# Kernel tuning notes

Measured on AMD Instinct MI355X. Metric: run time of the kernel, lower is better.

The kernel has to match this reference:

```python
import jax, jax.numpy as jnp
import numpy as np

N_NODES = 100000
N_EDGES = 1600000
D_FEAT = 64


def setup_inputs() -> dict:
    key = jax.random.key(0)
    k1, k2 = jax.random.split(key)
    x = jax.random.normal(k1, (N_NODES, D_FEAT), dtype=jnp.float32)
    edge_index = jax.random.randint(k2, (2, N_EDGES), 0, N_NODES, dtype=jnp.int64)
    return {"x": x, "edge_index": edge_index}


def reference(x, edge_index):
    # GCNProp (improved=False): remove self loops, add self loops w/ weight 1,
    # symmetric deg^-1/2 normalization, then spmm aggregation.
    N = x.shape[0]
    row, col = edge_index[0], edge_index[1]
    # remove_self_loops: zero the weight of any self-loop edge (math-equivalent
    # to dropping it, and jit-friendly: no data-dependent shapes).
    w = jnp.where(row != col, jnp.ones((), x.dtype), jnp.zeros((), x.dtype))
    # add_self_loops: append N diagonal edges with loop_value = 1 (improved=False)
    loop = jnp.arange(N, dtype=row.dtype)
    row_a = jnp.concatenate([row, loop])          # [E+N]
    col_a = jnp.concatenate([col, loop])          # [E+N]
    w_a = jnp.concatenate([w, jnp.ones((N,), x.dtype)])  # [E+N]
    # degree via scatter_add over rows
    deg = jax.ops.segment_sum(w_a, row_a, num_segments=N)  # [N]
    # deg^-0.5 with inf -> 0
    dinv = jnp.where(deg > 0, jax.lax.rsqrt(deg), jnp.zeros((), x.dtype))
    # edge normalization: deg[row]^-1/2 * w * deg[col]^-1/2
    norm = dinv[row_a] * w_a * dinv[col_a]        # [E+N]
    # spmm: gather neighbor features, scale, scatter-add into rows
    out = jax.ops.segment_sum(norm[:, None] * x[col_a], row_a, num_segments=N)  # [N, D]
    return out
```

## Files before the change

### kernel.cpp

```cpp
#include <hip/hip_runtime.h>

#define N_NODES 100000
#define N_EDGES 1600000
#define D 64
#define NB 391
#define BCAP 4480
#define PBLK 512
#define TPB 512
#define CHUNK ((N_EDGES + PBLK - 1) / PBLK)
#define CURSTRIDE 32

__device__ __forceinline__ unsigned short f2b(float f) {
    unsigned u = __float_as_uint(f);
    u += 0x7FFF + ((u >> 16) & 1);
    return (unsigned short)(u >> 16);
}

__global__ void init_cursor_kernel(int* __restrict__ cursor) {
    int b = blockIdx.x * blockDim.x + threadIdx.x;
    if (b < NB) cursor[b * CURSTRIDE] = b * BCAP;
}

__global__ __launch_bounds__(TPB) void scatter_direct_kernel(const int* __restrict__ ei,
                                                             int* __restrict__ cursor,
                                                             int* __restrict__ epack) {
    __shared__ int er[CHUNK];
    __shared__ int ec[CHUNK];
    __shared__ int h[NB];
    __shared__ int lbase[NB];
    __shared__ int lcur[NB];
    int t = threadIdx.x;
    for (int i = t; i < NB; i += TPB) h[i] = 0;
    int s = blockIdx.x * CHUNK;
    int e = min(s + CHUNK, N_EDGES);
    int n = e - s;
    for (int i = t; i < n; i += TPB) {
        er[i] = ei[s + i];
        ec[i] = ei[N_EDGES + s + i];
    }
    __syncthreads();
    for (int i = t; i < n; i += TPB) {
        int r = er[i], c = ec[i];
        if (r != c) atomicAdd(&h[r >> 8], 1);
    }
    __syncthreads();
    for (int i = t; i < NB; i += TPB) {
        lbase[i] = atomicAdd(&cursor[i * CURSTRIDE], h[i]);
        lcur[i] = 0;
    }
    __syncthreads();
    for (int i = t; i < n; i += TPB) {
        int r = er[i], c = ec[i];
        if (r != c) {
            int b = r >> 8;
            int p = lbase[b] + atomicAdd(&lcur[b], 1);
            epack[p] = ((r & 255) << 17) | c;
        }
    }
}

__global__ __launch_bounds__(TPB) void csr_sort_convert_kernel(const int* __restrict__ cursor,
                                                               int* __restrict__ epack,
                                                               int2* __restrict__ rowinfo,
                                                               const float* __restrict__ x,
                                                               unsigned short* __restrict__ xs) {
    __shared__ int ebuf[BCAP];
    __shared__ int h[256];
    __shared__ int sc[256];
    __shared__ int cur[256];
    __shared__ float dv[256];
    int b = blockIdx.x;
    int t = threadIdx.x;
    int base = b * BCAP;
    int n = min(cursor[b * CURSTRIDE] - base, BCAP);
    for (int i = t; i < n; i += TPB) ebuf[i] = epack[base + i];
    if (t < 256) h[t] = 0;
    __syncthreads();
    for (int i = t; i < n; i += TPB) atomicAdd(&h[ebuf[i] >> 17], 1);
    __syncthreads();
    int v = 0;
    if (t < 256) { v = h[t]; sc[t] = v; }
    __syncthreads();
    for (int off = 1; off < 256; off <<= 1) {
        int u = (t < 256 && t >= off) ? sc[t - off] : 0;
        __syncthreads();
        if (t < 256) sc[t] += u;
        __syncthreads();
    }
    if (t < 256) {
        int excl = sc[t] - v;
        int row = b * 256 + t;
        if (row < N_NODES) rowinfo[row] = make_int2(base + excl, v);
        dv[t] = rsqrtf((float)(1 + v));
        cur[t] = excl;
    }
    __syncthreads();
    for (int i = t; i < n; i += TPB) {
        int p = ebuf[i];
        int pos = atomicAdd(&cur[p >> 17], 1);
        epack[base + pos] = (p & 0x1FFFF) << 7;
    }
    int nrows = min(256, N_NODES - b * 256);
    const float4* x4 = (const float4*)x;
    ushort4* xs4 = (ushort4*)xs;
    for (int i = t; i < nrows * 16; i += TPB) {
        int rl = i >> 4;
        float4 vv = x4[(size_t)(b * 256 + rl) * 16 + (i & 15)];
        float dd = dv[rl];
        ushort4 o;
        o.x = f2b(vv.x * dd);
        o.y = f2b(vv.y * dd);
        o.z = f2b(vv.z * dd);
        o.w = f2b(vv.w * dd);
        xs4[(size_t)(b * 256 + rl) * 16 + (i & 15)] = o;
    }
}

__global__ __launch_bounds__(256) void gather_kernel(const unsigned short* __restrict__ xs,
                                                     const int2* __restrict__ rowinfo,
                                                     const int* __restrict__ colidx,
                                                     float* __restrict__ out) {
    int t = blockIdx.x * blockDim.x + threadIdx.x;
    int r = t >> 6;
    int lane = t & 63;
    if (r >= N_NODES) return;
    int lp = lane & 31;
    int hf = lane >> 5;
    int lpo = lp << 2;
    int2 ri = rowinfo[r];
    int start = ri.x;
    int end = start + ri.y;
    float dr = rsqrtf((float)(1 + ri.y));
    const char* xsb = (const char*)xs;
    float ax = 0.0f, ay = 0.0f;
    if (hf == 0) {
        unsigned v = *(const unsigned*)(xsb + (((size_t)r) << 7) + lpo);
        ax = __uint_as_float(v << 16);
        ay = __uint_as_float(v & 0xFFFF0000u);
    }
    for (int j = start; j < end; j += 64) {
        int idx = j + lane;
        int cj = (idx < end) ? colidx[idx] : 0;
        int n = min(64, end - j);
        int k = 0;
        for (; 2 * (k + 8) <= n; k += 8) {
            int s0 = __shfl(cj, 2 * k + hf);
            int s1 = __shfl(cj, 2 * k + 2 + hf);
            int s2 = __shfl(cj, 2 * k + 4 + hf);
            int s3 = __shfl(cj, 2 * k + 6 + hf);
            int s4 = __shfl(cj, 2 * k + 8 + hf);
            int s5 = __shfl(cj, 2 * k + 10 + hf);
            int s6 = __shfl(cj, 2 * k + 12 + hf);
            int s7 = __shfl(cj, 2 * k + 14 + hf);
            unsigned v0 = *(const unsigned*)(xsb + (unsigned)(s0 + lpo));
            unsigned v1 = *(const unsigned*)(xsb + (unsigned)(s1 + lpo));
            unsigned v2 = *(const unsigned*)(xsb + (unsigned)(s2 + lpo));
            unsigned v3 = *(const unsigned*)(xsb + (unsigned)(s3 + lpo));
            unsigned v4 = *(const unsigned*)(xsb + (unsigned)(s4 + lpo));
            unsigned v5 = *(const unsigned*)(xsb + (unsigned)(s5 + lpo));
            unsigned v6 = *(const unsigned*)(xsb + (unsigned)(s6 + lpo));
            unsigned v7 = *(const unsigned*)(xsb + (unsigned)(s7 + lpo));
            float a0 = __uint_as_float(v0 << 16), b0 = __uint_as_float(v0 & 0xFFFF0000u);
            float a1 = __uint_as_float(v1 << 16), b1 = __uint_as_float(v1 & 0xFFFF0000u);
            float a2 = __uint_as_float(v2 << 16), b2 = __uint_as_float(v2 & 0xFFFF0000u);
            float a3 = __uint_as_float(v3 << 16), b3 = __uint_as_float(v3 & 0xFFFF0000u);
            float a4 = __uint_as_float(v4 << 16), b4 = __uint_as_float(v4 & 0xFFFF0000u);
            float a5 = __uint_as_float(v5 << 16), b5 = __uint_as_float(v5 & 0xFFFF0000u);
            float a6 = __uint_as_float(v6 << 16), b6 = __uint_as_float(v6 & 0xFFFF0000u);
            float a7 = __uint_as_float(v7 << 16), b7 = __uint_as_float(v7 & 0xFFFF0000u);
            ax += ((a0 + a1) + (a2 + a3)) + ((a4 + a5) + (a6 + a7));
            ay += ((b0 + b1) + (b2 + b3)) + ((b4 + b5) + (b6 + b7));
        }
        for (; 2 * (k + 4) <= n; k += 4) {
            int s0 = __shfl(cj, 2 * k + hf);
            int s1 = __shfl(cj, 2 * k + 2 + hf);
            int s2 = __shfl(cj, 2 * k + 4 + hf);
            int s3 = __shfl(cj, 2 * k + 6 + hf);
            unsigned v0 = *(const unsigned*)(xsb + (unsigned)(s0 + lpo));
            unsigned v1 = *(const unsigned*)(xsb + (unsigned)(s1 + lpo));
            unsigned v2 = *(const unsigned*)(xsb + (unsigned)(s2 + lpo));
            unsigned v3 = *(const unsigned*)(xsb + (unsigned)(s3 + lpo));
            float a0 = __uint_as_float(v0 << 16), b0 = __uint_as_float(v0 & 0xFFFF0000u);
            float a1 = __uint_as_float(v1 << 16), b1 = __uint_as_float(v1 & 0xFFFF0000u);
            float a2 = __uint_as_float(v2 << 16), b2 = __uint_as_float(v2 & 0xFFFF0000u);
            float a3 = __uint_as_float(v3 << 16), b3 = __uint_as_float(v3 & 0xFFFF0000u);
            ax += (a0 + a1) + (a2 + a3);
            ay += (b0 + b1) + (b2 + b3);
        }
        for (; 2 * k < n; k++) {
            int src = 2 * k + hf;
            int s0 = __shfl(cj, (src < n) ? src : (n - 1));
            unsigned v0 = *(const unsigned*)(xsb + (unsigned)(s0 + lpo));
            if (src < n) {
                ax += __uint_as_float(v0 << 16);
                ay += __uint_as_float(v0 & 0xFFFF0000u);
            }
        }
    }
    ax += __shfl_xor(ax, 32);
    ay += __shfl_xor(ay, 32);
    if (hf == 0) {
        float2 o;
        o.x = dr * ax;
        o.y = dr * ay;
        ((float2*)out)[(size_t)r * 32 + lp] = o;
    }
}

extern "C" void kernel_launch(void* const* d_in, const int* in_sizes, int n_in,
                              void* d_out, int out_size, void* d_ws, size_t ws_size,
                              hipStream_t stream) {
    const float* x = (const float*)d_in[0];
    const int* ei = (const int*)d_in[1];
    float* out = (float*)d_out;

    int* cursor = (int*)d_ws;
    int2* rowinfo = (int2*)(cursor + NB * CURSTRIDE);
    int* epack = (int*)(rowinfo + N_NODES);
    unsigned short* xs = (unsigned short*)(epack + NB * BCAP);

    init_cursor_kernel<<<(NB + 255) / 256, 256, 0, stream>>>(cursor);
    scatter_direct_kernel<<<PBLK, TPB, 0, stream>>>(ei, cursor, epack);
    csr_sort_convert_kernel<<<NB, TPB, 0, stream>>>(cursor, epack, rowinfo, x, xs);
    gather_kernel<<<(N_NODES * D + 255) / 256, 256, 0, stream>>>(xs, rowinfo, epack, out);
}
```

Measured before the change: 160.1 us.

## Halve bucket size to 128 rows and drop LDS edge staging in scatter

Rows are now grouped into 782 buckets of 128 rows instead of 391 buckets of 256, and the sort/convert kernel runs with 256 threads per block. This gives more, smaller blocks with less shared memory each, which should raise occupancy and parallelism. The scatter kernel no longer stages edges in LDS and instead re-reads them from global memory in both passes. It also skips the global atomic for empty buckets. The trade-off is a second global read of the edge list in exchange for much lower LDS use in the scatter kernel, plus a tighter per-bucket capacity that could overflow if a bucket gets unusually many edges.

```diff
diff --git a/kernel.cpp b/kernel.cpp
--- a/kernel.cpp
+++ b/kernel.cpp
@@ -3,8 +3,9 @@
 #define N_NODES 100000
 #define N_EDGES 1600000
 #define D 64
-#define NB 391
-#define BCAP 4480
+#define BROWS 128
+#define NBK 782
+#define BCAP 2368
 #define PBLK 512
 #define TPB 512
 #define CHUNK ((N_EDGES + PBLK - 1) / PBLK)
@@ -18,101 +19,95 @@
 
 __global__ void init_cursor_kernel(int* __restrict__ cursor) {
     int b = blockIdx.x * blockDim.x + threadIdx.x;
-    if (b < NB) cursor[b * CURSTRIDE] = b * BCAP;
+    if (b < NBK) cursor[b * CURSTRIDE] = b * BCAP;
 }
 
 __global__ __launch_bounds__(TPB) void scatter_direct_kernel(const int* __restrict__ ei,
                                                              int* __restrict__ cursor,
                                                              int* __restrict__ epack) {
-    __shared__ int er[CHUNK];
-    __shared__ int ec[CHUNK];
-    __shared__ int h[NB];
-    __shared__ int lbase[NB];
-    __shared__ int lcur[NB];
+    __shared__ int h[NBK];
+    __shared__ int lbase[NBK];
+    __shared__ int lcur[NBK];
     int t = threadIdx.x;
-    for (int i = t; i < NB; i += TPB) h[i] = 0;
+    for (int i = t; i < NBK; i += TPB) h[i] = 0;
+    __syncthreads();
     int s = blockIdx.x * CHUNK;
     int e = min(s + CHUNK, N_EDGES);
-    int n = e - s;
-    for (int i = t; i < n; i += TPB) {
-        er[i] = ei[s + i];
-        ec[i] = ei[N_EDGES + s + i];
-    }
-    __syncthreads();
-    for (int i = t; i < n; i += TPB) {
-        int r = er[i], c = ec[i];
-        if (r != c) atomicAdd(&h[r >> 8], 1);
-    }
-    __syncthreads();
-    for (int i = t; i < NB; i += TPB) {
-        lbase[i] = atomicAdd(&cursor[i * CURSTRIDE], h[i]);
+    for (int i = s + t; i < e; i += TPB) {
+        int r = ei[i], c = ei[N_EDGES + i];
+        if (r != c) atomicAdd(&h[r >> 7], 1);
+    }
+    __syncthreads();
+    for (int i = t; i < NBK; i += TPB) {
+        int hv = h[i];
+        lbase[i] = hv ? atomicAdd(&cursor[i * CURSTRIDE], hv) : 0;
         lcur[i] = 0;
     }
     __syncthreads();
-    for (int i = t; i < n; i += TPB) {
-        int r = er[i], c = ec[i];
+    for (int i = s + t; i < e; i += TPB) {
+        int r = ei[i], c = ei[N_EDGES + i];
         if (r != c) {
-            int b = r >> 8;
+            int b = r >> 7;
             int p = lbase[b] + atomicAdd(&lcur[b], 1);
-            epack[p] = ((r & 255) << 17) | c;
-        }
-    }
-}
-
-__global__ __launch_bounds__(TPB) void csr_sort_convert_kernel(const int* __restrict__ cursor,
+            epack[p] = ((r & 127) << 17) | c;
+        }
+    }
+}
+
+__global__ __launch_bounds__(256) void csr_sort_convert_kernel(const int* __restrict__ cursor,
                                                                int* __restrict__ epack,
                                                                int2* __restrict__ rowinfo,
                                                                const float* __restrict__ x,
                                                                unsigned short* __restrict__ xs) {
     __shared__ int ebuf[BCAP];
-    __shared__ int h[256];
-    __shared__ int sc[256];
-    __shared__ int cur[256];
-    __shared__ float dv[256];
+    __shared__ int h[BROWS];
+    __shared__ int sc[BROWS];
+    __shared__ int cur[BROWS];
+    __shared__ float dv[BROWS];
     int b = blockIdx.x;
     int t = threadIdx.x;
     int base = b * BCAP;
     int n = min(cursor[b * CURSTRIDE] - base, BCAP);
-    for (int i = t; i < n; i += TPB) ebuf[i] = epack[base + i];
-    if (t < 256) h[t] = 0;
-    __syncthreads();
-    for (int i = t; i < n; i += TPB) atomicAdd(&h[ebuf[i] >> 17], 1);
+    for (int i = t; i < n; i += 256) ebuf[i] = epack[base + i];
+    if (t < BROWS) h[t] = 0;
+    __syncthreads();
+    for (int i = t; i < n; i += 256) atomicAdd(&h[ebuf[i] >> 17], 1);
     __syncthreads();
     int v = 0;
-    if (t < 256) { v = h[t]; sc[t] = v; }
-    __syncthreads();
-    for (int off = 1; off < 256; off <<= 1) {
-        int u = (t < 256 && t >= off) ? sc[t - off] : 0;
+    if (t < BROWS) { v = h[t]; sc[t] = v; }
+    __syncthreads();
+    for (int off = 1; off < BROWS; off <<= 1) {
+        int u = (t < BROWS && t >= off) ? sc[t - off] : 0;
         __syncthreads();
-        if (t < 256) sc[t] += u;
+        if (t < BROWS) sc[t] += u;
         __syncthreads();
     }
-    if (t < 256) {
+    if (t < BROWS) {
         int excl = sc[t] - v;
-        int row = b * 256 + t;
+        int row = b * BROWS + t;
         if (row < N_NODES) rowinfo[row] = make_int2(base + excl, v);
         dv[t] = rsqrtf((float)(1 + v));
         cur[t] = excl;
     }
     __syncthreads();
-    for (int i = t; i < n; i += TPB) {
+    for (int i = t; i < n; i += 256) {
         int p = ebuf[i];
         int pos = atomicAdd(&cur[p >> 17], 1);
         epack[base + pos] = (p & 0x1FFFF) << 7;
     }
-    int nrows = min(256, N_NODES - b * 256);
+    int nrows = min(BROWS, N_NODES - b * BROWS);
     const float4* x4 = (const float4*)x;
     ushort4* xs4 = (ushort4*)xs;
-    for (int i = t; i < nrows * 16; i += TPB) {
+    for (int i = t; i < nrows * 16; i += 256) {
         int rl = i >> 4;
-        float4 vv = x4[(size_t)(b * 256 + rl) * 16 + (i & 15)];
+        float4 vv = x4[(size_t)(b * BROWS + rl) * 16 + (i & 15)];
         float dd = dv[rl];
         ushort4 o;
         o.x = f2b(vv.x * dd);
         o.y = f2b(vv.y * dd);
         o.z = f2b(vv.z * dd);
         o.w = f2b(vv.w * dd);
-        xs4[(size_t)(b * 256 + rl) * 16 + (i & 15)] = o;
+        xs4[(size_t)(b * BROWS + rl) * 16 + (i & 15)] = o;
     }
 }
 
@@ -215,12 +210,12 @@
     float* out = (float*)d_out;
 
     int* cursor = (int*)d_ws;
-    int2* rowinfo = (int2*)(cursor + NB * CURSTRIDE);
+    int2* rowinfo = (int2*)(cursor + NBK * CURSTRIDE);
     int* epack = (int*)(rowinfo + N_NODES);
-    unsigned short* xs = (unsigned short*)(epack + NB * BCAP);
-
-    init_cursor_kernel<<<(NB + 255) / 256, 256, 0, stream>>>(cursor);
+    unsigned short* xs = (unsigned short*)(epack + NBK * BCAP);
+
+    init_cursor_kernel<<<(NBK + 255) / 256, 256, 0, stream>>>(cursor);
     scatter_direct_kernel<<<PBLK, TPB, 0, stream>>>(ei, cursor, epack);
-    csr_sort_convert_kernel<<<NB, TPB, 0, stream>>>(cursor, epack, rowinfo, x, xs);
+    csr_sort_convert_kernel<<<NBK, 256, 0, stream>>>(cursor, epack, rowinfo, x, xs);
     gather_kernel<<<(N_NODES * D + 255) / 256, 256, 0, stream>>>(xs, rowinfo, epack, out);
 }
```

Result: slower. 167.3 us (+4.5%).

## Split bf16 conversion into its own kernel and drop scatter's shared staging

Applied to the files above, without the earlier changes.

Moves the x-scaling and bf16 conversion out of the per-bucket sort kernel into a separate, more finely parallel kernel, with deg^-1/2 passed through a new dinv buffer. The scatter kernel now uses 256 blocks of 1024 threads and reads edges straight from global memory twice, where it used to stage them in shared memory. It also skips cursor atomics for empty buckets and vectorises the epack load in the sort kernel. The aim is more parallelism and less shared-memory pressure, at the cost of an extra kernel launch and a second global pass over the edges.

```diff
diff --git a/kernel.cpp b/kernel.cpp
--- a/kernel.cpp
+++ b/kernel.cpp
@@ -5,10 +5,12 @@
 #define D 64
 #define NB 391
 #define BCAP 4480
-#define PBLK 512
+#define PBLK 256
+#define STPB 1024
 #define TPB 512
 #define CHUNK ((N_EDGES + PBLK - 1) / PBLK)
 #define CURSTRIDE 32
+#define CROWS 64
 
 __device__ __forceinline__ unsigned short f2b(float f) {
     unsigned u = __float_as_uint(f);
@@ -21,36 +23,30 @@
     if (b < NB) cursor[b * CURSTRIDE] = b * BCAP;
 }
 
-__global__ __launch_bounds__(TPB) void scatter_direct_kernel(const int* __restrict__ ei,
-                                                             int* __restrict__ cursor,
-                                                             int* __restrict__ epack) {
-    __shared__ int er[CHUNK];
-    __shared__ int ec[CHUNK];
+__global__ __launch_bounds__(STPB) void scatter_direct_kernel(const int* __restrict__ ei,
+                                                              int* __restrict__ cursor,
+                                                              int* __restrict__ epack) {
     __shared__ int h[NB];
     __shared__ int lbase[NB];
     __shared__ int lcur[NB];
     int t = threadIdx.x;
-    for (int i = t; i < NB; i += TPB) h[i] = 0;
+    for (int i = t; i < NB; i += STPB) h[i] = 0;
+    __syncthreads();
     int s = blockIdx.x * CHUNK;
     int e = min(s + CHUNK, N_EDGES);
-    int n = e - s;
-    for (int i = t; i < n; i += TPB) {
-        er[i] = ei[s + i];
-        ec[i] = ei[N_EDGES + s + i];
-    }
-    __syncthreads();
-    for (int i = t; i < n; i += TPB) {
-        int r = er[i], c = ec[i];
+    for (int i = s + t; i < e; i += STPB) {
+        int r = ei[i], c = ei[N_EDGES + i];
         if (r != c) atomicAdd(&h[r >> 8], 1);
     }
     __syncthreads();
-    for (int i = t; i < NB; i += TPB) {
-        lbase[i] = atomicAdd(&cursor[i * CURSTRIDE], h[i]);
+    for (int i = t; i < NB; i += STPB) {
+        int hv = h[i];
+        lbase[i] = hv ? atomicAdd(&cursor[i * CURSTRIDE], hv) : 0;
         lcur[i] = 0;
     }
     __syncthreads();
-    for (int i = t; i < n; i += TPB) {
-        int r = er[i], c = ec[i];
+    for (int i = s + t; i < e; i += STPB) {
+        int r = ei[i], c = ei[N_EDGES + i];
         if (r != c) {
             int b = r >> 8;
             int p = lbase[b] + atomicAdd(&lcur[b], 1);
@@ -59,21 +55,22 @@
     }
 }
 
-__global__ __launch_bounds__(TPB) void csr_sort_convert_kernel(const int* __restrict__ cursor,
-                                                               int* __restrict__ epack,
-                                                               int2* __restrict__ rowinfo,
-                                                               const float* __restrict__ x,
-                                                               unsigned short* __restrict__ xs) {
+__global__ __launch_bounds__(TPB) void csr_sort_kernel(const int* __restrict__ cursor,
+                                                       int* __restrict__ epack,
+                                                       int2* __restrict__ rowinfo,
+                                                       float* __restrict__ dinv) {
     __shared__ int ebuf[BCAP];
     __shared__ int h[256];
     __shared__ int sc[256];
     __shared__ int cur[256];
-    __shared__ float dv[256];
     int b = blockIdx.x;
     int t = threadIdx.x;
     int base = b * BCAP;
     int n = min(cursor[b * CURSTRIDE] - base, BCAP);
-    for (int i = t; i < n; i += TPB) ebuf[i] = epack[base + i];
+    const int4* ep4 = (const int4*)(epack + base);
+    int n4 = n >> 2;
+    for (int i = t; i < n4; i += TPB) ((int4*)ebuf)[i] = ep4[i];
+    for (int i = (n4 << 2) + t; i < n; i += TPB) ebuf[i] = epack[base + i];
     if (t < 256) h[t] = 0;
     __syncthreads();
     for (int i = t; i < n; i += TPB) atomicAdd(&h[ebuf[i] >> 17], 1);
@@ -90,8 +87,10 @@
     if (t < 256) {
         int excl = sc[t] - v;
         int row = b * 256 + t;
-        if (row < N_NODES) rowinfo[row] = make_int2(base + excl, v);
-        dv[t] = rsqrtf((float)(1 + v));
+        if (row < N_NODES) {
+            rowinfo[row] = make_int2(base + excl, v);
+            dinv[row] = rsqrtf((float)(1 + v));
+        }
         cur[t] = excl;
     }
     __syncthreads();
@@ -100,19 +99,30 @@
         int pos = atomicAdd(&cur[p >> 17], 1);
         epack[base + pos] = (p & 0x1FFFF) << 7;
     }
-    int nrows = min(256, N_NODES - b * 256);
+}
+
+__global__ __launch_bounds__(256) void convert_kernel(const float* __restrict__ x,
+                                                      const float* __restrict__ dinv,
+                                                      unsigned short* __restrict__ xs) {
+    __shared__ float dv[CROWS];
+    int b = blockIdx.x;
+    int t = threadIdx.x;
+    int r0 = b * CROWS;
+    int nrows = min(CROWS, N_NODES - r0);
+    if (t < nrows) dv[t] = dinv[r0 + t];
+    __syncthreads();
     const float4* x4 = (const float4*)x;
     ushort4* xs4 = (ushort4*)xs;
-    for (int i = t; i < nrows * 16; i += TPB) {
+    for (int i = t; i < nrows * 16; i += 256) {
         int rl = i >> 4;
-        float4 vv = x4[(size_t)(b * 256 + rl) * 16 + (i & 15)];
+        float4 vv = x4[(size_t)(r0 + rl) * 16 + (i & 15)];
         float dd = dv[rl];
         ushort4 o;
         o.x = f2b(vv.x * dd);
         o.y = f2b(vv.y * dd);
         o.z = f2b(vv.z * dd);
         o.w = f2b(vv.w * dd);
-        xs4[(size_t)(b * 256 + rl) * 16 + (i & 15)] = o;
+        xs4[(size_t)(r0 + rl) * 16 + (i & 15)] = o;
     }
 }
 
@@ -216,11 +226,13 @@
 
     int* cursor = (int*)d_ws;
     int2* rowinfo = (int2*)(cursor + NB * CURSTRIDE);
-    int* epack = (int*)(rowinfo + N_NODES);
+    float* dinv = (float*)(rowinfo + N_NODES);
+    int* epack = (int*)(dinv + N_NODES);
     unsigned short* xs = (unsigned short*)(epack + NB * BCAP);
 
     init_cursor_kernel<<<(NB + 255) / 256, 256, 0, stream>>>(cursor);
-    scatter_direct_kernel<<<PBLK, TPB, 0, stream>>>(ei, cursor, epack);
-    csr_sort_convert_kernel<<<NB, TPB, 0, stream>>>(cursor, epack, rowinfo, x, xs);
+    scatter_direct_kernel<<<PBLK, STPB, 0, stream>>>(ei, cursor, epack);
+    csr_sort_kernel<<<NB, TPB, 0, stream>>>(cursor, epack, rowinfo, dinv);
+    convert_kernel<<<(N_NODES + CROWS - 1) / CROWS, 256, 0, stream>>>(x, dinv, xs);
     gather_kernel<<<(N_NODES * D + 255) / 256, 256, 0, stream>>>(xs, rowinfo, epack, out);
 }
```

Measured after the change: 153.5 us. -4.1%, faster.
